# Performance work log

Measured on AMD Instinct MI355X. Metric: run time of the kernel, lower is better.

The kernel has to match this reference:

```python
import jax, jax.numpy as jnp
import numpy as np

POOLED = 7          # square pooled grid (grid_width == grid_height required by torch_combined_meshgrid)
NUM_LEVELS = 6      # len_feature_maps; level = clamp(floor(5 + log2(sqrt(w*h))), 0, 5)


def _bilinear_sample(fm, gx, gy):
    """fm: [C, D, D]; gx, gy: [N, G, G] normalized coords in [0,1].
    Faithful to getWeightedSum_ofFourFmapPoints: floor/ceil corner points with
    proportion weights; coord dim 0 (x) indexes fmap rows, dim 1 (y) indexes cols.
    Returns [N, C, G, G]."""
    D = fm.shape[-1]
    ux = gx * (D - 1)
    uy = gy * (D - 1)
    x0 = jnp.floor(ux); x1 = jnp.ceil(ux)
    y0 = jnp.floor(uy); y1 = jnp.ceil(uy)
    ddx = jnp.where(x1 - x0 == 0, 1.0, x1 - x0)
    ddy = jnp.where(y1 - y0 == 0, 1.0, y1 - y0)
    px0 = 1.0 - (ux - x0) / ddx   # proportion_to_take_from_start_x
    px1 = 1.0 - px0
    py0 = 1.0 - (uy - y0) / ddy
    py1 = 1.0 - py0
    ix0 = x0.astype(jnp.int32); ix1 = x1.astype(jnp.int32)
    iy0 = y0.astype(jnp.int32); iy1 = y1.astype(jnp.int32)
    # advanced indexing: fm[:, idx, idx] -> [C, N, G, G]
    tl = fm[:, ix0, iy0]
    tr = fm[:, ix1, iy0]
    bl = fm[:, ix0, iy1]
    br = fm[:, ix1, iy1]
    w_tl = (px0 * py0)[None]
    w_tr = (px1 * py0)[None]
    w_bl = (px0 * py1)[None]
    w_br = (px1 * py1)[None]
    pooled = w_tl * tl + w_tr * tr + w_bl * bl + w_br * br  # [C, N, G, G]
    return jnp.moveaxis(pooled, 0, 1)                        # [N, C, G, G]


def setup_inputs() -> dict:
    key = jax.random.key(0)
    N, C = 2000, 256
    dims = [38, 19, 10, 5, 3, 1]
    kw, kh, kx, ky, *kf = jax.random.split(key, 4 + len(dims))
    w = jax.random.uniform(kw, (N, 1), minval=0.02, maxval=0.98)
    h = jax.random.uniform(kh, (N, 1), minval=0.02, maxval=0.98)
    x1 = jax.random.uniform(kx, (N, 1)) * (1.0 - w)
    y1 = jax.random.uniform(ky, (N, 1)) * (1.0 - h)
    boxes = jnp.concatenate([x1, y1, x1 + w, y1 + h], axis=1)  # x1 y1 x2 y2 in [0,1]
    out = {"boxes": boxes}
    for i, (d, k) in enumerate(zip(dims, kf)):
        out[f"fmap{i}"] = jax.random.normal(k, (1, C, d, d), dtype=jnp.float32)
    return out


def reference(boxes, fmap0, fmap1, fmap2, fmap3, fmap4, fmap5):
    fmaps = [fmap0, fmap1, fmap2, fmap3, fmap4, fmap5]
    N = boxes.shape[0]
    C = fmap0.shape[1]
    G = POOLED
    x1, y1, x2, y2 = boxes[:, 0:1], boxes[:, 1:2], boxes[:, 2:3], boxes[:, 3:4]
    # FPN-style level index: floor(5 + log2(sqrt(w*h))), clamped (constant w.r.t. grad)
    avg = jnp.sqrt((x2 - x1) * (y2 - y1))
    lvl = jnp.clip(jnp.floor((NUM_LEVELS - 1.0) + jnp.log2(avg)), 0, NUM_LEVELS - 1)
    lvl = jax.lax.stop_gradient(lvl.astype(jnp.int32).reshape(-1))  # [N]
    # bilinear interpolation grid: grid[n,i,j] = (x1 + i*dx/(G-1), y1 + j*dy/(G-1)), clamped
    t = jnp.arange(G, dtype=boxes.dtype)
    denom = max(1.0, G - 1.0)
    xr = jnp.clip(x1 + t[None, :] * (x2 - x1) / denom, 0.0, 1.0)  # [N, G]
    yr = jnp.clip(y1 + t[None, :] * (y2 - y1) / denom, 0.0, 1.0)  # [N, G]
    gx = jnp.broadcast_to(xr[:, :, None], (N, G, G))
    gy = jnp.broadcast_to(yr[:, None, :], (N, G, G))
    out = jnp.zeros((N, C, G, G), dtype=fmap0.dtype)
    for l, f in enumerate(fmaps):
        fm = f[0]  # [C, D, D] (single image; one fmap selected per box)
        if fm.shape[-1] == 1:
            # original returns fmap[:, :, 0:1, 0:1]; broadcast the constant to the grid
            pooled = jnp.broadcast_to(fm[None, :, :1, :1], (N, C, G, G))
        else:
            pooled = _bilinear_sample(fm, gx, gy)
        mask = (lvl == l).astype(fmap0.dtype)[:, None, None, None]
        out = out + mask * pooled
    return out
```

## Files before the change

kernel.cpp:

```cpp
#include <hip/hip_runtime.h>

#define G 7
#define CCH 256
#define NLVL 6

typedef float vfloat4 __attribute__((ext_vector_type(4)));

__device__ __constant__ int kD[NLVL]  = {38, 19, 10, 5, 3, 1};
__device__ __constant__ int kD2[NLVL] = {1444, 361, 100, 25, 9, 1};
__device__ __constant__ int kBaseT[NLVL + 1] = {0, 369664, 462080, 487680, 494080, 496384, 496640};

#define FMT_TOTAL 496640

#define RL_F(v, l) __builtin_bit_cast(float, __builtin_amdgcn_readlane(__builtin_bit_cast(int, (v)), (l)))
#define RL_I(v, l) __builtin_amdgcn_readlane((v), (l))

__global__ __launch_bounds__(256) void transpose_fmaps(
    const float* __restrict__ f0, const float* __restrict__ f1,
    const float* __restrict__ f2, const float* __restrict__ f3,
    const float* __restrict__ f4, const float* __restrict__ f5,
    float* __restrict__ fmT)
{
    int o = blockIdx.x * blockDim.x + threadIdx.x;
    if (o >= FMT_TOTAL) return;
    int l = 0;
#pragma unroll
    for (int k = 1; k < NLVL; ++k) l += (o >= kBaseT[k]);
    int rel = o - kBaseT[l];
    int p = rel >> 8;
    int c = rel & 255;
    const float* f;
    switch (l) {
        case 0: f = f0; break;
        case 1: f = f1; break;
        case 2: f = f2; break;
        case 3: f = f3; break;
        case 4: f = f4; break;
        default: f = f5; break;
    }
    fmT[o] = f[c * kD2[l] + p];
}

__global__ __launch_bounds__(256) void roialign_main(
    const float* __restrict__ boxes, const float* __restrict__ fmT,
    float* __restrict__ out)
{
    __shared__ float sOut[CCH * 49];

    int n = blockIdx.x;
    int tid = threadIdx.x;
    int lane = tid & 63;

    float bx1 = boxes[n * 4 + 0];
    float by1 = boxes[n * 4 + 1];
    float bx2 = boxes[n * 4 + 2];
    float by2 = boxes[n * 4 + 3];
    float w = bx2 - bx1;
    float h = by2 - by1;
    float avg = sqrtf(w * h);
    float lf = floorf((float)(NLVL - 1) + log2f(avg));
    lf = fminf(fmaxf(lf, 0.0f), (float)(NLVL - 1));
    int lvl = __builtin_amdgcn_readfirstlane((int)lf);
    int D    = kD[lvl];
    int base = kBaseT[lvl];
    float Dm1 = (float)(D - 1);
    int Dm1i = D - 1;
    int Drow = D << 8;

    float t = (float)lane;
    float xr = fminf(fmaxf(bx1 + (t * w) / 6.0f, 0.0f), 1.0f);
    float ux = xr * Dm1;
    float xf = floorf(ux);
    float fxv = ux - xf;
    int ix0 = (int)xf;
    int xoAv = ix0 * Drow;
    int xoBv = xoAv + ((ix0 < Dm1i) ? Drow : 0);
    float xpAv = 1.0f - fxv;

    float yr = fminf(fmaxf(by1 + (t * h) / 6.0f, 0.0f), 1.0f);
    float uy = yr * Dm1;
    float yf = floorf(uy);
    float fyv = uy - yf;
    int iy0 = (int)yf;
    int yoAv = iy0 << 8;
    int yoBv = yoAv + ((iy0 < Dm1i) ? 256 : 0);
    float ypAv = 1.0f - fyv;

    float xwA[7], xwB[7], ywA[7], ywB[7];
    int   xoA[7], xoB[7], yoA[7], yoB[7];
#pragma unroll
    for (int k = 0; k < 7; ++k) {
        xwA[k] = RL_F(xpAv, k);
        xwB[k] = RL_F(fxv, k);
        xoA[k] = RL_I(xoAv, k);
        xoB[k] = RL_I(xoBv, k);
        ywA[k] = RL_F(ypAv, k);
        ywB[k] = RL_F(fyv, k);
        yoA[k] = RL_I(yoAv, k);
        yoB[k] = RL_I(yoBv, k);
    }

    const float* fmB = fmT + base;
    float* row = sOut + tid * 49;

#pragma unroll
    for (int i = 0; i < 7; ++i) {
        float sxA = xwA[i], sxB = xwB[i];
        const float* pA = fmB + xoA[i];
        const float* pB = fmB + xoB[i];
#pragma unroll
        for (int j = 0; j < 7; ++j) {
            float syA = ywA[j], syB = ywB[j];
            const float* q00 = pA + yoA[j];
            const float* q10 = pB + yoA[j];
            const float* q01 = pA + yoB[j];
            const float* q11 = pB + yoB[j];
            float a00 = q00[tid];
            float a10 = q10[tid];
            float a01 = q01[tid];
            float a11 = q11[tid];
            float vx0 = sxA * a00 + sxB * a10;
            float vx1 = sxA * a01 + sxB * a11;
            row[i * 7 + j] = syA * vx0 + syB * vx1;
        }
    }

    asm volatile("s_waitcnt lgkmcnt(0)" ::: "memory");
    __builtin_amdgcn_sched_barrier(0);

    int wv_id = tid >> 6;
    const vfloat4* s4 = (const vfloat4*)sOut + wv_id * 784;
    vfloat4* out4 = (vfloat4*)(out + (size_t)n * (CCH * G * G)) + wv_id * 784;
#pragma unroll
    for (int k = 0; k < 12; ++k) {
        __builtin_nontemporal_store(s4[k * 64 + lane], &out4[k * 64 + lane]);
    }
    if (lane < 16) {
        __builtin_nontemporal_store(s4[768 + lane], &out4[768 + lane]);
    }
}

__global__ __launch_bounds__(256) void roialign_fallback(
    const float* __restrict__ boxes,
    const float* __restrict__ f0, const float* __restrict__ f1,
    const float* __restrict__ f2, const float* __restrict__ f3,
    const float* __restrict__ f4, const float* __restrict__ f5,
    float* __restrict__ out, int total4)
{
    int t = blockIdx.x * blockDim.x + threadIdx.x;
    if (t >= total4) return;
    const int perN = CCH * G * G;
    int idx = t * 4;
    int n = idx / perN;
    int rem = idx - n * perN;
    float bx1 = boxes[n * 4 + 0], by1 = boxes[n * 4 + 1];
    float bx2 = boxes[n * 4 + 2], by2 = boxes[n * 4 + 3];
    float w = bx2 - bx1, h = by2 - by1;
    float avg = sqrtf(w * h);
    float lf = floorf((float)(NLVL - 1) + log2f(avg));
    lf = fminf(fmaxf(lf, 0.0f), (float)(NLVL - 1));
    int lvl = (int)lf;
    const float* fm;
    switch (lvl) {
        case 0: fm = f0; break;
        case 1: fm = f1; break;
        case 2: fm = f2; break;
        case 3: fm = f3; break;
        case 4: fm = f4; break;
        default: fm = f5; break;
    }
    int D = kD[lvl];
    float Dm1 = (float)(D - 1);
    float4 res;
    float* rp = &res.x;
#pragma unroll
    for (int k = 0; k < 4; ++k) {
        int e = rem + k;
        int j = e % G;
        int iq = e / G;
        int i = iq % G;
        int c = iq / G;
        float xr = fminf(fmaxf(bx1 + ((float)i * w) / 6.0f, 0.0f), 1.0f);
        float yr = fminf(fmaxf(by1 + ((float)j * h) / 6.0f, 0.0f), 1.0f);
        float ux = xr * Dm1, uy = yr * Dm1;
        float x0 = floorf(ux), y0 = floorf(uy);
        int ix0 = (int)x0, iy0 = (int)y0;
        float fx = ux - x0, fy = uy - y0;
        int ix1 = min(ix0 + 1, D - 1), iy1 = min(iy0 + 1, D - 1);
        const float* p = fm + c * D * D;
        float v00 = p[ix0 * D + iy0], v10 = p[ix1 * D + iy0];
        float v01 = p[ix0 * D + iy1], v11 = p[ix1 * D + iy1];
        float px0 = 1.0f - fx, py0 = 1.0f - fy;
        rp[k] = px0 * py0 * v00 + fx * py0 * v10 + px0 * fy * v01 + fx * fy * v11;
    }
    reinterpret_cast<float4*>(out)[t] = res;
}

extern "C" void kernel_launch(void* const* d_in, const int* in_sizes, int n_in,
                              void* d_out, int out_size, void* d_ws, size_t ws_size,
                              hipStream_t stream) {
    const float* boxes = (const float*)d_in[0];
    const float* f0 = (const float*)d_in[1];
    const float* f1 = (const float*)d_in[2];
    const float* f2 = (const float*)d_in[3];
    const float* f3 = (const float*)d_in[4];
    const float* f4 = (const float*)d_in[5];
    const float* f5 = (const float*)d_in[6];
    float* out = (float*)d_out;
    int N = in_sizes[0] / 4;

    if (ws_size >= (size_t)FMT_TOTAL * sizeof(float)) {
        float* fmT = (float*)d_ws;
        transpose_fmaps<<<(FMT_TOTAL + 255) / 256, 256, 0, stream>>>(
            f0, f1, f2, f3, f4, f5, fmT);
        roialign_main<<<N, 256, 0, stream>>>(boxes, fmT, out);
    } else {
        int total4 = out_size / 4;
        roialign_fallback<<<(total4 + 255) / 256, 256, 0, stream>>>(
            boxes, f0, f1, f2, f3, f4, f5, out, total4);
    }
}
```

Baseline: 29.50 us.

## Pack horizontally adjacent fmap pairs as float2 to halve gather loads

The preprocessing kernel now writes, for each channel-last fmap entry, a float2 holding the value and its y+1 neighbour (clamped at the edge). The main kernel then issues two 8-byte loads per output sample instead of four 4-byte loads, which cuts load instructions and address arithmetic in the gather loop. The cost is a workspace twice as large, which doubles the write traffic of the pack kernel and the footprint the main kernel reads from cache.

```diff
diff --git a/kernel.cpp b/kernel.cpp
--- a/kernel.cpp
+++ b/kernel.cpp
@@ -10,25 +10,29 @@
 __device__ __constant__ int kD2[NLVL] = {1444, 361, 100, 25, 9, 1};
 __device__ __constant__ int kBaseT[NLVL + 1] = {0, 369664, 462080, 487680, 494080, 496384, 496640};
 
-#define FMT_TOTAL 496640
+#define FMT2_ENTRIES 496640
 
 #define RL_F(v, l) __builtin_bit_cast(float, __builtin_amdgcn_readlane(__builtin_bit_cast(int, (v)), (l)))
 #define RL_I(v, l) __builtin_amdgcn_readlane((v), (l))
 
-__global__ __launch_bounds__(256) void transpose_fmaps(
+__global__ __launch_bounds__(256) void pack_fmaps(
     const float* __restrict__ f0, const float* __restrict__ f1,
     const float* __restrict__ f2, const float* __restrict__ f3,
     const float* __restrict__ f4, const float* __restrict__ f5,
-    float* __restrict__ fmT)
+    float2* __restrict__ fmT2)
 {
     int o = blockIdx.x * blockDim.x + threadIdx.x;
-    if (o >= FMT_TOTAL) return;
+    if (o >= FMT2_ENTRIES) return;
     int l = 0;
 #pragma unroll
     for (int k = 1; k < NLVL; ++k) l += (o >= kBaseT[k]);
     int rel = o - kBaseT[l];
     int p = rel >> 8;
     int c = rel & 255;
+    int D = kD[l];
+    int x = p / D;
+    int y = p - x * D;
+    int y1 = min(y + 1, D - 1);
     const float* f;
     switch (l) {
         case 0: f = f0; break;
@@ -38,11 +42,12 @@
         case 4: f = f4; break;
         default: f = f5; break;
     }
-    fmT[o] = f[c * kD2[l] + p];
+    const float* fc = f + c * kD2[l] + x * D;
+    fmT2[o] = make_float2(fc[y], fc[y1]);
 }
 
 __global__ __launch_bounds__(256) void roialign_main(
-    const float* __restrict__ boxes, const float* __restrict__ fmT,
+    const float* __restrict__ boxes, const float2* __restrict__ fm2,
     float* __restrict__ out)
 {
     __shared__ float sOut[CCH * 49];
@@ -62,10 +67,9 @@
     lf = fminf(fmaxf(lf, 0.0f), (float)(NLVL - 1));
     int lvl = __builtin_amdgcn_readfirstlane((int)lf);
     int D    = kD[lvl];
-    int base = kBaseT[lvl];
     float Dm1 = (float)(D - 1);
     int Dm1i = D - 1;
-    int Drow = D << 8;
+    int DrowE = D << 8;
 
     float t = (float)lane;
     float xr = fminf(fmaxf(bx1 + (t * w) / 6.0f, 0.0f), 1.0f);
@@ -73,8 +77,8 @@
     float xf = floorf(ux);
     float fxv = ux - xf;
     int ix0 = (int)xf;
-    int xoAv = ix0 * Drow;
-    int xoBv = xoAv + ((ix0 < Dm1i) ? Drow : 0);
+    int xoAv = ix0 * DrowE;
+    int xoBv = min(ix0 + 1, Dm1i) * DrowE;
     float xpAv = 1.0f - fxv;
 
     float yr = fminf(fmaxf(by1 + (t * h) / 6.0f, 0.0f), 1.0f);
@@ -82,12 +86,11 @@
     float yf = floorf(uy);
     float fyv = uy - yf;
     int iy0 = (int)yf;
-    int yoAv = iy0 << 8;
-    int yoBv = yoAv + ((iy0 < Dm1i) ? 256 : 0);
+    int yov = iy0 << 8;
     float ypAv = 1.0f - fyv;
 
     float xwA[7], xwB[7], ywA[7], ywB[7];
-    int   xoA[7], xoB[7], yoA[7], yoB[7];
+    int   xoA[7], xoB[7], yo[7];
 #pragma unroll
     for (int k = 0; k < 7; ++k) {
         xwA[k] = RL_F(xpAv, k);
@@ -96,32 +99,24 @@
         xoB[k] = RL_I(xoBv, k);
         ywA[k] = RL_F(ypAv, k);
         ywB[k] = RL_F(fyv, k);
-        yoA[k] = RL_I(yoAv, k);
-        yoB[k] = RL_I(yoBv, k);
-    }
-
-    const float* fmB = fmT + base;
+        yo[k]  = RL_I(yov, k);
+    }
+
+    const float2* fmB = fm2 + kBaseT[lvl] + tid;
     float* row = sOut + tid * 49;
 
 #pragma unroll
     for (int i = 0; i < 7; ++i) {
         float sxA = xwA[i], sxB = xwB[i];
-        const float* pA = fmB + xoA[i];
-        const float* pB = fmB + xoB[i];
+        const float2* pA = fmB + xoA[i];
+        const float2* pB = fmB + xoB[i];
 #pragma unroll
         for (int j = 0; j < 7; ++j) {
-            float syA = ywA[j], syB = ywB[j];
-            const float* q00 = pA + yoA[j];
-            const float* q10 = pB + yoA[j];
-            const float* q01 = pA + yoB[j];
-            const float* q11 = pB + yoB[j];
-            float a00 = q00[tid];
-            float a10 = q10[tid];
-            float a01 = q01[tid];
-            float a11 = q11[tid];
-            float vx0 = sxA * a00 + sxB * a10;
-            float vx1 = sxA * a01 + sxB * a11;
-            row[i * 7 + j] = syA * vx0 + syB * vx1;
+            float2 a = pA[yo[j]];
+            float2 b = pB[yo[j]];
+            float vx0 = sxA * a.x + sxB * b.x;
+            float vx1 = sxA * a.y + sxB * b.y;
+            row[i * 7 + j] = ywA[j] * vx0 + ywB[j] * vx1;
         }
     }
 
@@ -209,11 +204,11 @@
     float* out = (float*)d_out;
     int N = in_sizes[0] / 4;
 
-    if (ws_size >= (size_t)FMT_TOTAL * sizeof(float)) {
-        float* fmT = (float*)d_ws;
-        transpose_fmaps<<<(FMT_TOTAL + 255) / 256, 256, 0, stream>>>(
-            f0, f1, f2, f3, f4, f5, fmT);
-        roialign_main<<<N, 256, 0, stream>>>(boxes, fmT, out);
+    if (ws_size >= (size_t)FMT2_ENTRIES * sizeof(float2)) {
+        float2* fmT2 = (float2*)d_ws;
+        pack_fmaps<<<(FMT2_ENTRIES + 255) / 256, 256, 0, stream>>>(
+            f0, f1, f2, f3, f4, f5, fmT2);
+        roialign_main<<<N, 256, 0, stream>>>(boxes, fmT2, out);
     } else {
         int total4 = out_size / 4;
         roialign_fallback<<<(total4 + 255) / 256, 256, 0, stream>>>(
```

Result: slower. 39.22 us (+33.0%).
